# Kernel optimization log

Hardware: AMD Instinct MI355X
Metric: run time of the kernel (lower is better)

## Reference

```python
import jax, jax.numpy as jnp
import numpy as np

N_HEAD = 4

def setup_inputs() -> dict:
    key = jax.random.key(0)
    ks = jax.random.split(key, 10)
    B, N, C = 4, 16384, 256
    s = 1.0 / np.sqrt(C)
    inp = {
        'x': jax.random.normal(ks[0], (B, N, C), dtype=jnp.float32),
        'mask_x': jnp.ones((B, N), dtype=jnp.float32),
        'mask_y': jnp.ones((B, N), dtype=jnp.float32),
        'Wq': jax.random.normal(ks[1], (C, C), dtype=jnp.float32) * s,
        'bq': jnp.zeros((C,), dtype=jnp.float32),
        'Wk': jax.random.normal(ks[2], (C, C), dtype=jnp.float32) * s,
        'bk': jnp.zeros((C,), dtype=jnp.float32),
        'Wv': jax.random.normal(ks[3], (C, C), dtype=jnp.float32) * s,
        'bv': jnp.zeros((C,), dtype=jnp.float32),
        'Wp': jax.random.normal(ks[4], (C, C), dtype=jnp.float32) * s,
        'bp': jnp.zeros((C,), dtype=jnp.float32),
    }
    return inp

def reference(x, mask_x, mask_y, Wq, bq, Wk, bk, Wv, bv, Wp, bp):
    B, N, C = x.shape
    H = N_HEAD
    D = C // H
    # projections (y = x, self-attention path); weights stored [in, out]
    def split_heads(t):  # [B,N,C] -> [B,H,N,D]
        return t.reshape(B, N, H, D).transpose(0, 2, 1, 3)
    Q = split_heads(x @ Wq + bq)
    K = split_heads(x @ Wk + bk)
    V = split_heads(x @ Wv + bv)
    mx = mask_x[:, None, :, None]  # [B,1,N,1]
    my = mask_y[:, None, :, None]  # [B,1,M,1]
    K = K * my
    V = V * my
    # torch F.gelu default is exact (erf) gelu
    Q = jax.nn.gelu(Q, approximate=False) + 1.0
    K = jax.nn.gelu(K, approximate=False) + 1.0
    KV = jnp.einsum('bhmd,bhme->bhde', K, V)          # [B,H,D,D]
    K_sum = K.sum(axis=2, keepdims=True)               # [B,H,1,D]
    denom = jnp.sum(Q * K_sum, axis=-1, keepdims=True) # [B,H,N,1]
    attn_out = jnp.einsum('bhnd,bhde->bhne', Q, KV) / denom
    attn_out = attn_out * mx
    out = attn_out.transpose(0, 2, 1, 3).reshape(B, N, C)
    return out @ Wp + bp
```

## Files before the change

kernel.cpp:

```cpp
#include <hip/hip_runtime.h>
#include <hip/hip_bf16.h>
#include <cstdint>
#include <cstddef>

#define SEQ   16384
#define CHN   256

typedef __attribute__((ext_vector_type(8))) short  short8;
typedef __attribute__((ext_vector_type(4))) float  f32x4;

#define AS1 __attribute__((address_space(1)))
#define AS3 __attribute__((address_space(3)))
static __device__ __forceinline__ void gl_lds16(const void* g, void* l) {
    __builtin_amdgcn_global_load_lds((const AS1 void*)g, (AS3 void*)l, 16, 0, 0);
}

static __device__ __forceinline__ unsigned short f2bf(float f) {
    unsigned int u = __builtin_bit_cast(unsigned int, f);
    u += 0x7fffu + ((u >> 16) & 1u);
    return (unsigned short)(u >> 16);
}
static __device__ __forceinline__ float bf2f(unsigned short h) {
    unsigned int u = ((unsigned int)h) << 16;
    return __builtin_bit_cast(float, u);
}
static __device__ __forceinline__ float gelu_exact(float x) {
    return 0.5f * x * (1.0f + erff(x * 0.70710678118654752f));
}
static __device__ __forceinline__ int swz_us(int row, int kbyte) {
    return (row * 128 + (kbyte ^ ((row & 7) << 4))) >> 1;
}

__global__ __launch_bounds__(256) void cvt_kernel(
    const float* __restrict__ x, unsigned short* __restrict__ xb)
{
    const int t0 = blockIdx.x * 256 + threadIdx.x;
    #pragma unroll
    for (int i = 0; i < 4; ++i) {
        const long g = (long)t0 + (long)i * 524288;
        const float4 a = *(const float4*)(x + g * 8);
        const float4 b = *(const float4*)(x + g * 8 + 4);
        uint4 pk;
        pk.x = (unsigned int)f2bf(a.x) | ((unsigned int)f2bf(a.y) << 16);
        pk.y = (unsigned int)f2bf(a.z) | ((unsigned int)f2bf(a.w) << 16);
        pk.z = (unsigned int)f2bf(b.x) | ((unsigned int)f2bf(b.y) << 16);
        pk.w = (unsigned int)f2bf(b.z) | ((unsigned int)f2bf(b.w) << 16);
        *(uint4*)(xb + g * 8) = pk;
    }
}

__global__ __launch_bounds__(256) void prep_kernel(
    const float* __restrict__ Wq, const float* __restrict__ Wk,
    const float* __restrict__ Wv, const float* __restrict__ Wp,
    unsigned short* __restrict__ Wcat, unsigned short* __restrict__ Wpt,
    float* __restrict__ KV, float* __restrict__ Ksum)
{
    const int idx = blockIdx.x * 256 + threadIdx.x;
    const int n = idx >> 8, k = idx & 255;
    const int src = k * 256 + n;
    Wcat[idx]          = f2bf(Wq[src]);
    Wcat[65536 + idx]  = f2bf(Wk[src]);
    Wcat[131072 + idx] = f2bf(Wv[src]);
    Wpt[idx]           = f2bf(Wp[src]);
    KV[idx] = 0.0f;
    if (idx < 1024) Ksum[idx] = 0.0f;
}

__global__ __launch_bounds__(256) void qkv_gemm(
    const unsigned short* __restrict__ xb, const float* __restrict__ my,
    const unsigned short* __restrict__ Wcat,
    const float* __restrict__ bq, const float* __restrict__ bk,
    const float* __restrict__ bv,
    unsigned short* __restrict__ Qb, unsigned short* __restrict__ Kb,
    unsigned short* __restrict__ Vb)
{
    __shared__ unsigned short As[128 * 64];
    __shared__ unsigned short Bs[128 * 64];
    __shared__ float mys[128];
    const int t = threadIdx.x;
    const int nwg = 3072, phys = blockIdx.x;
    const int l = (phys & 7) * (nwg >> 3) + (phys >> 3);
    const int rt = l / 6, ct = l % 6;
    const long row0 = (long)rt * 128;
    const int  ncol0 = ct * 128;
    const int  mat = ct >> 1;
    const int lane = t & 63, wave = t >> 6, wm = wave >> 1, wn = wave & 1;

    if (t < 128) mys[t] = my[row0 + t];

    f32x4 acc[4][4];
    #pragma unroll
    for (int i = 0; i < 4; ++i)
        #pragma unroll
        for (int j = 0; j < 4; ++j) acc[i][j] = (f32x4)0.0f;

    for (int k0 = 0; k0 < 256; k0 += 64) {
        #pragma unroll
        for (int i = 0; i < 4; ++i) {
            const int c = i * 256 + t;
            gl_lds16(xb + (row0 + (c >> 3)) * 256 + k0 + (c & 7) * 8, &As[c * 8]);
        }
        #pragma unroll
        for (int i = 0; i < 4; ++i) {
            const int c = i * 256 + t;
            gl_lds16(Wcat + (size_t)(ncol0 + (c >> 3)) * 256 + k0 + (c & 7) * 8, &Bs[c * 8]);
        }
        __syncthreads();
        #pragma unroll
        for (int kk = 0; kk < 2; ++kk) {
            short8 af[4], bfr[4];
            #pragma unroll
            for (int mi = 0; mi < 4; ++mi) {
                const int r = wm * 64 + mi * 16 + (lane & 15);
                af[mi] = *(const short8*)&As[r * 64 + kk * 32 + (lane >> 4) * 8];
            }
            #pragma unroll
            for (int ni = 0; ni < 4; ++ni) {
                const int n = wn * 64 + ni * 16 + (lane & 15);
                bfr[ni] = *(const short8*)&Bs[n * 64 + kk * 32 + (lane >> 4) * 8];
            }
            #pragma unroll
            for (int mi = 0; mi < 4; ++mi)
                #pragma unroll
                for (int ni = 0; ni < 4; ++ni)
                    acc[mi][ni] = __builtin_amdgcn_mfma_f32_16x16x32_bf16(
                        af[mi], bfr[ni], acc[mi][ni], 0, 0, 0);
        }
        __syncthreads();
    }

    const float* bias  = (mat == 0) ? bq : (mat == 1) ? bk : bv;
    unsigned short* Ob = (mat == 0) ? Qb : (mat == 1) ? Kb : Vb;
    const int col0 = (ct & 1) * 128;
    #pragma unroll
    for (int ni = 0; ni < 4; ++ni) {
        const int coll = col0 + wn * 64 + ni * 16 + (lane & 15);
        const float bc = bias[coll];
        #pragma unroll
        for (int mi = 0; mi < 4; ++mi) {
            const int lr0 = wm * 64 + mi * 16 + ((lane >> 4) << 2);
            #pragma unroll
            for (int r = 0; r < 4; ++r) {
                const int lr = lr0 + r;
                float val = acc[mi][ni][r] + bc;
                if (mat == 0)      val = gelu_exact(val) + 1.0f;
                else if (mat == 1) val = gelu_exact(val * mys[lr]) + 1.0f;
                else               val = val * mys[lr];
                Ob[(row0 + lr) * 256 + coll] = f2bf(val);
            }
        }
    }
}

__global__ __launch_bounds__(256) void kv_reduce(
    const unsigned short* __restrict__ Kb, const unsigned short* __restrict__ Vb,
    float* __restrict__ KV, float* __restrict__ Ksum)
{
    __shared__ float kf[16][64];
    __shared__ float vf[16][64];
    const int t = threadIdx.x;
    const int bh = blockIdx.y;
    const long base = (long)(bh >> 2) * SEQ * 256 + (bh & 3) * 64;
    const long m0 = (long)blockIdx.x * 256;
    const int d0 = (t >> 4) * 4, e0 = (t & 15) * 4;
    const int sr = t >> 4, swhich = (t >> 3) & 1, sseg = t & 7;
    float acc[4][4] = {};
    float ks[4] = {};
    for (int it = 0; it < 16; ++it) {
        const long row = m0 + it * 16 + sr;
        const unsigned short* src = (swhich ? Vb : Kb) + base + row * 256 + sseg * 8;
        const uint4 raw = *(const uint4*)src;
        const unsigned short* rh = (const unsigned short*)&raw;
        float* dst = swhich ? &vf[sr][sseg * 8] : &kf[sr][sseg * 8];
        #pragma unroll
        for (int j = 0; j < 8; ++j) dst[j] = bf2f(rh[j]);
        __syncthreads();
        #pragma unroll
        for (int mm = 0; mm < 16; ++mm) {
            const float4 kd = *(const float4*)&kf[mm][d0];
            const float4 ve = *(const float4*)&vf[mm][e0];
            const float k4[4] = {kd.x, kd.y, kd.z, kd.w};
            const float v4[4] = {ve.x, ve.y, ve.z, ve.w};
            #pragma unroll
            for (int i = 0; i < 4; ++i)
                #pragma unroll
                for (int j = 0; j < 4; ++j) acc[i][j] += k4[i] * v4[j];
            if ((t & 15) == 0) {
                #pragma unroll
                for (int i = 0; i < 4; ++i) ks[i] += k4[i];
            }
        }
        __syncthreads();
    }
    #pragma unroll
    for (int i = 0; i < 4; ++i)
        #pragma unroll
        for (int j = 0; j < 4; ++j)
            atomicAdd(&KV[((size_t)bh * 64 + d0 + i) * 64 + e0 + j], acc[i][j]);
    if ((t & 15) == 0) {
        #pragma unroll
        for (int i = 0; i < 4; ++i) atomicAdd(&Ksum[bh * 64 + d0 + i], ks[i]);
    }
}

__global__ __launch_bounds__(256) void attn_kernel(
    const unsigned short* __restrict__ Qb, const float* __restrict__ KV,
    const float* __restrict__ Ksum, const float* __restrict__ mx,
    unsigned short* __restrict__ Ab)
{
    __shared__ unsigned short Qs[128 * 64];
    __shared__ unsigned short KVT[64 * 64];
    __shared__ float ksh[64];
    __shared__ float sden[128];
    const int t = threadIdx.x;
    const long row0 = (long)blockIdx.x * 128;
    const int b = (int)(row0 >> 14);
    const int lane = t & 63, wave = t >> 6, wm = wave >> 1, wn = wave & 1;

    for (int h = 0; h < 4; ++h) {
        const int bh = b * 4 + h;
        #pragma unroll
        for (int it = 0; it < 4; ++it) {
            const int idx = it * 256 + t;
            const int r = idx >> 3, c8 = (idx & 7) * 8;
            const uint4 v = *(const uint4*)(Qb + (row0 + r) * 256 + h * 64 + c8);
            *(uint4*)&Qs[swz_us(r, c8 * 2)] = v;
        }
        {
            const int e = t & 63, dg = t >> 6;
            #pragma unroll
            for (int i = 0; i < 16; ++i) {
                const int d = dg * 16 + i;
                const float v = KV[((size_t)bh * 64 + d) * 64 + e];
                KVT[(e * 128 + ((d * 2) ^ ((e & 7) << 4))) >> 1] = f2bf(v);
            }
        }
        if (t < 64) ksh[t] = Ksum[bh * 64 + t];
        __syncthreads();
        if (t < 128) {
            float s = 0.0f;
            for (int d = 0; d < 64; ++d)
                s += bf2f(Qs[swz_us(t, d * 2)]) * ksh[d];
            sden[t] = mx[row0 + t] / s;
        }
        __syncthreads();
        f32x4 acc[4][2];
        #pragma unroll
        for (int i = 0; i < 4; ++i) { acc[i][0] = (f32x4)0.0f; acc[i][1] = (f32x4)0.0f; }
        #pragma unroll
        for (int kk = 0; kk < 2; ++kk) {
            const int kbyte = kk * 64 + (lane >> 4) * 16;
            short8 af[4], bfr[2];
            #pragma unroll
            for (int mi = 0; mi < 4; ++mi) {
                const int r = wm * 64 + mi * 16 + (lane & 15);
                af[mi] = *(const short8*)&Qs[swz_us(r, kbyte)];
            }
            #pragma unroll
            for (int ni = 0; ni < 2; ++ni) {
                const int e = wn * 32 + ni * 16 + (lane & 15);
                bfr[ni] = *(const short8*)&KVT[swz_us(e, kbyte)];
            }
            #pragma unroll
            for (int mi = 0; mi < 4; ++mi)
                #pragma unroll
                for (int ni = 0; ni < 2; ++ni)
                    acc[mi][ni] = __builtin_amdgcn_mfma_f32_16x16x32_bf16(
                        af[mi], bfr[ni], acc[mi][ni], 0, 0, 0);
        }
        #pragma unroll
        for (int ni = 0; ni < 2; ++ni) {
            const int e = wn * 32 + ni * 16 + (lane & 15);
            #pragma unroll
            for (int mi = 0; mi < 4; ++mi) {
                const int lr0 = wm * 64 + mi * 16 + ((lane >> 4) << 2);
                #pragma unroll
                for (int r = 0; r < 4; ++r) {
                    const int lr = lr0 + r;
                    const float val = acc[mi][ni][r] * sden[lr];
                    Ab[(row0 + lr) * 256 + h * 64 + e] = f2bf(val);
                }
            }
        }
        __syncthreads();
    }
}

__global__ __launch_bounds__(256) void proj_gemm(
    const unsigned short* __restrict__ Ab, const unsigned short* __restrict__ Wpt,
    const float* __restrict__ bp, float* __restrict__ out)
{
    __shared__ unsigned short As[128 * 64];
    __shared__ unsigned short Bs[128 * 64];
    const int t = threadIdx.x;
    const int nwg = 1024, phys = blockIdx.x;
    const int l = (phys & 7) * (nwg >> 3) + (phys >> 3);
    const int rt = l >> 1, ct = l & 1;
    const long row0 = (long)rt * 128;
    const int col0 = ct * 128;
    const int lane = t & 63, wave = t >> 6, wm = wave >> 1, wn = wave & 1;

    f32x4 acc[4][4];
    #pragma unroll
    for (int i = 0; i < 4; ++i)
        #pragma unroll
        for (int j = 0; j < 4; ++j) acc[i][j] = (f32x4)0.0f;

    for (int k0 = 0; k0 < 256; k0 += 64) {
        #pragma unroll
        for (int i = 0; i < 4; ++i) {
            const int c = i * 256 + t;
            gl_lds16(Ab + (row0 + (c >> 3)) * 256 + k0 + (c & 7) * 8, &As[c * 8]);
        }
        #pragma unroll
        for (int i = 0; i < 4; ++i) {
            const int c = i * 256 + t;
            gl_lds16(Wpt + (size_t)(col0 + (c >> 3)) * 256 + k0 + (c & 7) * 8, &Bs[c * 8]);
        }
        __syncthreads();
        #pragma unroll
        for (int kk = 0; kk < 2; ++kk) {
            short8 af[4], bfr[4];
            #pragma unroll
            for (int mi = 0; mi < 4; ++mi) {
                const int r = wm * 64 + mi * 16 + (lane & 15);
                af[mi] = *(const short8*)&As[r * 64 + kk * 32 + (lane >> 4) * 8];
            }
            #pragma unroll
            for (int ni = 0; ni < 4; ++ni) {
                const int n = wn * 64 + ni * 16 + (lane & 15);
                bfr[ni] = *(const short8*)&Bs[n * 64 + kk * 32 + (lane >> 4) * 8];
            }
            #pragma unroll
            for (int mi = 0; mi < 4; ++mi)
                #pragma unroll
                for (int ni = 0; ni < 4; ++ni)
                    acc[mi][ni] = __builtin_amdgcn_mfma_f32_16x16x32_bf16(
                        af[mi], bfr[ni], acc[mi][ni], 0, 0, 0);
        }
        __syncthreads();
    }
    #pragma unroll
    for (int ni = 0; ni < 4; ++ni) {
        const int coll = col0 + wn * 64 + ni * 16 + (lane & 15);
        const float bc = bp[coll];
        #pragma unroll
        for (int mi = 0; mi < 4; ++mi) {
            const int lr0 = wm * 64 + mi * 16 + ((lane >> 4) << 2);
            #pragma unroll
            for (int r = 0; r < 4; ++r) {
                const long grow = row0 + lr0 + r;
                out[grow * 256 + coll] = acc[mi][ni][r] + bc;
            }
        }
    }
}

extern "C" void kernel_launch(void* const* d_in, const int* in_sizes, int n_in,
                              void* d_out, int out_size, void* d_ws, size_t ws_size,
                              hipStream_t stream)
{
    (void)in_sizes; (void)n_in; (void)out_size; (void)ws_size;
    const float* x  = (const float*)d_in[0];
    const float* mx = (const float*)d_in[1];
    const float* my = (const float*)d_in[2];
    const float* Wq = (const float*)d_in[3];
    const float* bq = (const float*)d_in[4];
    const float* Wk = (const float*)d_in[5];
    const float* bk = (const float*)d_in[6];
    const float* Wv = (const float*)d_in[7];
    const float* bv = (const float*)d_in[8];
    const float* Wp = (const float*)d_in[9];
    const float* bp = (const float*)d_in[10];
    float* out = (float*)d_out;

    const size_t nelem = (size_t)4 * SEQ * CHN;
    char* w = (char*)d_ws;
    unsigned short* xb   = (unsigned short*)w; w += nelem * 2;
    unsigned short* Qb   = (unsigned short*)w; w += nelem * 2;
    unsigned short* Kb   = (unsigned short*)w; w += nelem * 2;
    unsigned short* Vb   = (unsigned short*)w; w += nelem * 2;
    unsigned short* Wcat = (unsigned short*)w; w += 768 * 256 * 2;
    unsigned short* Wpt  = (unsigned short*)w; w += 131072;
    float* KV   = (float*)w; w += 262144;
    float* Ksum = (float*)w; w += 4096;
    unsigned short* Ab = Kb;

    cvt_kernel<<<2048, 256, 0, stream>>>(x, xb);
    prep_kernel<<<256, 256, 0, stream>>>(Wq, Wk, Wv, Wp, Wcat, Wpt, KV, Ksum);
    qkv_gemm<<<3072, 256, 0, stream>>>(xb, my, Wcat, bq, bk, bv, Qb, Kb, Vb);
    kv_reduce<<<dim3(64, 16), 256, 0, stream>>>(Kb, Vb, KV, Ksum);
    attn_kernel<<<512, 256, 0, stream>>>(Qb, KV, Ksum, mx, Ab);
    proj_gemm<<<1024, 256, 0, stream>>>(Ab, Wpt, bp, out);
}
```

Before: 349.9 us.

## Double-buffer and swizzle GEMMs, transpose K/V, compute KV with MFMA

The QKV and projection GEMMs now double-buffer their LDS tiles and use an XOR swizzle, so loads overlap MFMA work and LDS bank conflicts drop. The QKV epilogue stages results in LDS and writes vectorized rows; K and V are written transposed as [B,H,D,N]. This lets the KV reduction run as an MFMA GEMM instead of a scalar FP32 outer-product loop. The attention denominator is also computed with vectorized loads over all threads. The cost is more LDS per block and a transposed-store epilogue.

After: 338.1 us. 3.4% less time.

```diff
diff --git a/kernel.cpp b/kernel.cpp
--- a/kernel.cpp
+++ b/kernel.cpp
@@ -71,11 +71,11 @@
     const unsigned short* __restrict__ Wcat,
     const float* __restrict__ bq, const float* __restrict__ bk,
     const float* __restrict__ bv,
-    unsigned short* __restrict__ Qb, unsigned short* __restrict__ Kb,
-    unsigned short* __restrict__ Vb)
-{
-    __shared__ unsigned short As[128 * 64];
-    __shared__ unsigned short Bs[128 * 64];
+    unsigned short* __restrict__ Qb, unsigned short* __restrict__ Kt,
+    unsigned short* __restrict__ Vt)
+{
+    __shared__ unsigned short As[2][128 * 64];
+    __shared__ unsigned short Bs[2][128 * 64];
     __shared__ float mys[128];
     const int t = threadIdx.x;
     const int nwg = 3072, phys = blockIdx.x;
@@ -84,40 +84,52 @@
     const long row0 = (long)rt * 128;
     const int  ncol0 = ct * 128;
     const int  mat = ct >> 1;
+    const int  col0 = (ct & 1) * 128;
     const int lane = t & 63, wave = t >> 6, wm = wave >> 1, wn = wave & 1;
 
-    if (t < 128) mys[t] = my[row0 + t];
-
-    f32x4 acc[4][4];
-    #pragma unroll
-    for (int i = 0; i < 4; ++i)
-        #pragma unroll
-        for (int j = 0; j < 4; ++j) acc[i][j] = (f32x4)0.0f;
-
-    for (int k0 = 0; k0 < 256; k0 += 64) {
+    auto stage = [&](int buf, int k0) {
         #pragma unroll
         for (int i = 0; i < 4; ++i) {
             const int c = i * 256 + t;
-            gl_lds16(xb + (row0 + (c >> 3)) * 256 + k0 + (c & 7) * 8, &As[c * 8]);
+            const int row = c >> 3, j = (c & 7) ^ (row & 7);
+            gl_lds16(xb + (row0 + row) * 256 + k0 + j * 8, &As[buf][c * 8]);
         }
         #pragma unroll
         for (int i = 0; i < 4; ++i) {
             const int c = i * 256 + t;
-            gl_lds16(Wcat + (size_t)(ncol0 + (c >> 3)) * 256 + k0 + (c & 7) * 8, &Bs[c * 8]);
-        }
-        __syncthreads();
+            const int row = c >> 3, j = (c & 7) ^ (row & 7);
+            gl_lds16(Wcat + (size_t)(ncol0 + row) * 256 + k0 + j * 8, &Bs[buf][c * 8]);
+        }
+    };
+
+    if (t < 128) mys[t] = my[row0 + t];
+
+    f32x4 acc[4][4];
+    #pragma unroll
+    for (int i = 0; i < 4; ++i)
+        #pragma unroll
+        for (int j = 0; j < 4; ++j) acc[i][j] = (f32x4)0.0f;
+
+    stage(0, 0);
+    __syncthreads();
+
+    #pragma unroll
+    for (int s = 0; s < 4; ++s) {
+        const int buf = s & 1;
+        if (s < 3) stage(buf ^ 1, (s + 1) * 64);
         #pragma unroll
         for (int kk = 0; kk < 2; ++kk) {
+            const int g = kk * 4 + (lane >> 4);
             short8 af[4], bfr[4];
             #pragma unroll
             for (int mi = 0; mi < 4; ++mi) {
                 const int r = wm * 64 + mi * 16 + (lane & 15);
-                af[mi] = *(const short8*)&As[r * 64 + kk * 32 + (lane >> 4) * 8];
+                af[mi] = *(const short8*)&As[buf][r * 64 + (g ^ (r & 7)) * 8];
             }
             #pragma unroll
             for (int ni = 0; ni < 4; ++ni) {
                 const int n = wn * 64 + ni * 16 + (lane & 15);
-                bfr[ni] = *(const short8*)&Bs[n * 64 + kk * 32 + (lane >> 4) * 8];
+                bfr[ni] = *(const short8*)&Bs[buf][n * 64 + (g ^ (n & 7)) * 8];
             }
             #pragma unroll
             for (int mi = 0; mi < 4; ++mi)
@@ -129,13 +141,12 @@
         __syncthreads();
     }
 
-    const float* bias  = (mat == 0) ? bq : (mat == 1) ? bk : bv;
-    unsigned short* Ob = (mat == 0) ? Qb : (mat == 1) ? Kb : Vb;
-    const int col0 = (ct & 1) * 128;
+    unsigned short* C = &As[0][0];
+    const float* bias = (mat == 0) ? bq : (mat == 1) ? bk : bv;
     #pragma unroll
     for (int ni = 0; ni < 4; ++ni) {
-        const int coll = col0 + wn * 64 + ni * 16 + (lane & 15);
-        const float bc = bias[coll];
+        const int cl = wn * 64 + ni * 16 + (lane & 15);
+        const float bc = bias[col0 + cl];
         #pragma unroll
         for (int mi = 0; mi < 4; ++mi) {
             const int lr0 = wm * 64 + mi * 16 + ((lane >> 4) << 2);
@@ -146,61 +157,71 @@
                 if (mat == 0)      val = gelu_exact(val) + 1.0f;
                 else if (mat == 1) val = gelu_exact(val * mys[lr]) + 1.0f;
                 else               val = val * mys[lr];
-                Ob[(row0 + lr) * 256 + coll] = f2bf(val);
-            }
-        }
-    }
-}
-
-__global__ __launch_bounds__(256) void kv_reduce(
-    const unsigned short* __restrict__ Kb, const unsigned short* __restrict__ Vb,
+                if (mat == 0) {
+                    C[lr * 128 + cl] = f2bf(val);
+                } else {
+                    C[(cl * 256 + ((lr * 2) ^ ((cl & 7) << 4))) >> 1] = f2bf(val);
+                }
+            }
+        }
+    }
+    __syncthreads();
+
+    if (mat == 0) {
+        const int r = t >> 1, c0 = (t & 1) * 64;
+        uint4* dst = (uint4*)(Qb + (row0 + r) * 256 + col0 + c0);
+        const uint4* src = (const uint4*)&C[r * 128 + c0];
+        #pragma unroll
+        for (int q = 0; q < 8; ++q) dst[q] = src[q];
+    } else {
+        const int chl = t >> 1, mh = (t & 1) * 64;
+        const int chg = col0 + chl, h = chg >> 6, d = chg & 63;
+        const int b = (int)(row0 >> 14);
+        const long m0 = (row0 & 16383) + mh;
+        unsigned short* dstp = (mat == 1 ? Kt : Vt)
+                             + ((size_t)(b * 4 + h) * 64 + d) * SEQ + m0;
+        #pragma unroll
+        for (int q = 0; q < 8; ++q) {
+            const int byteoff = chl * 256 + ((mh * 2 + q * 16) ^ ((chl & 7) << 4));
+            *(uint4*)(dstp + q * 8) = *(const uint4*)((const char*)C + byteoff);
+        }
+    }
+}
+
+__global__ __launch_bounds__(256) void kv_gemm(
+    const unsigned short* __restrict__ Kt, const unsigned short* __restrict__ Vt,
     float* __restrict__ KV, float* __restrict__ Ksum)
 {
-    __shared__ float kf[16][64];
-    __shared__ float vf[16][64];
-    const int t = threadIdx.x;
+    const int t = threadIdx.x, lane = t & 63, w = t >> 6;
     const int bh = blockIdx.y;
-    const long base = (long)(bh >> 2) * SEQ * 256 + (bh & 3) * 64;
-    const long m0 = (long)blockIdx.x * 256;
-    const int d0 = (t >> 4) * 4, e0 = (t & 15) * 4;
-    const int sr = t >> 4, swhich = (t >> 3) & 1, sseg = t & 7;
-    float acc[4][4] = {};
-    float ks[4] = {};
-    for (int it = 0; it < 16; ++it) {
-        const long row = m0 + it * 16 + sr;
-        const unsigned short* src = (swhich ? Vb : Kb) + base + row * 256 + sseg * 8;
-        const uint4 raw = *(const uint4*)src;
-        const unsigned short* rh = (const unsigned short*)&raw;
-        float* dst = swhich ? &vf[sr][sseg * 8] : &kf[sr][sseg * 8];
-        #pragma unroll
-        for (int j = 0; j < 8; ++j) dst[j] = bf2f(rh[j]);
-        __syncthreads();
-        #pragma unroll
-        for (int mm = 0; mm < 16; ++mm) {
-            const float4 kd = *(const float4*)&kf[mm][d0];
-            const float4 ve = *(const float4*)&vf[mm][e0];
-            const float k4[4] = {kd.x, kd.y, kd.z, kd.w};
-            const float v4[4] = {ve.x, ve.y, ve.z, ve.w};
-            #pragma unroll
-            for (int i = 0; i < 4; ++i)
-                #pragma unroll
-                for (int j = 0; j < 4; ++j) acc[i][j] += k4[i] * v4[j];
-            if ((t & 15) == 0) {
-                #pragma unroll
-                for (int i = 0; i < 4; ++i) ks[i] += k4[i];
-            }
-        }
-        __syncthreads();
-    }
-    #pragma unroll
-    for (int i = 0; i < 4; ++i)
+    const long k0 = (long)blockIdx.x * 512;
+    const unsigned short* Ka = Kt + ((size_t)bh * 64 + w * 16 + (lane & 15)) * SEQ;
+    f32x4 acc[4];
+    #pragma unroll
+    for (int e = 0; e < 4; ++e) acc[e] = (f32x4)0.0f;
+    float ksacc = 0.0f;
+
+    for (int ks = 0; ks < 16; ++ks) {
+        const long kk = k0 + ks * 32 + (lane >> 4) * 8;
+        const short8 a = *(const short8*)(Ka + kk);
+        #pragma unroll
+        for (int j = 0; j < 8; ++j) ksacc += bf2f((unsigned short)a[j]);
+        #pragma unroll
+        for (int e = 0; e < 4; ++e) {
+            const short8 b = *(const short8*)(Vt
+                + ((size_t)bh * 64 + e * 16 + (lane & 15)) * SEQ + kk);
+            acc[e] = __builtin_amdgcn_mfma_f32_16x16x32_bf16(a, b, acc[e], 0, 0, 0);
+        }
+    }
+    ksacc += __shfl_xor(ksacc, 16, 64);
+    ksacc += __shfl_xor(ksacc, 32, 64);
+    if (lane < 16) atomicAdd(&Ksum[bh * 64 + w * 16 + lane], ksacc);
+    #pragma unroll
+    for (int e = 0; e < 4; ++e)
         #pragma unroll
         for (int j = 0; j < 4; ++j)
-            atomicAdd(&KV[((size_t)bh * 64 + d0 + i) * 64 + e0 + j], acc[i][j]);
-    if ((t & 15) == 0) {
-        #pragma unroll
-        for (int i = 0; i < 4; ++i) atomicAdd(&Ksum[bh * 64 + d0 + i], ks[i]);
-    }
+            atomicAdd(&KV[((size_t)bh * 64 + w * 16 + (lane >> 4) * 4 + j) * 64
+                          + e * 16 + (lane & 15)], acc[e][j]);
 }
 
 __global__ __launch_bounds__(256) void attn_kernel(
@@ -237,11 +258,19 @@
         }
         if (t < 64) ksh[t] = Ksum[bh * 64 + t];
         __syncthreads();
-        if (t < 128) {
+        {
+            const int r = t >> 1, hf = t & 1;
             float s = 0.0f;
-            for (int d = 0; d < 64; ++d)
-                s += bf2f(Qs[swz_us(t, d * 2)]) * ksh[d];
-            sden[t] = mx[row0 + t] / s;
+            #pragma unroll
+            for (int c8 = 0; c8 < 4; ++c8) {
+                const int ke = hf * 32 + c8 * 8;
+                const short8 q8 = *(const short8*)&Qs[swz_us(r, ke * 2)];
+                #pragma unroll
+                for (int j = 0; j < 8; ++j)
+                    s += bf2f((unsigned short)q8[j]) * ksh[ke + j];
+            }
+            s += __shfl_xor(s, 1, 64);
+            if (hf == 0) sden[r] = mx[row0 + r] / s;
         }
         __syncthreads();
         f32x4 acc[4][2];
@@ -290,8 +319,8 @@
     const unsigned short* __restrict__ Ab, const unsigned short* __restrict__ Wpt,
     const float* __restrict__ bp, float* __restrict__ out)
 {
-    __shared__ unsigned short As[128 * 64];
-    __shared__ unsigned short Bs[128 * 64];
+    __shared__ unsigned short As[2][128 * 64];
+    __shared__ unsigned short Bs[2][128 * 64];
     const int t = threadIdx.x;
     const int nwg = 1024, phys = blockIdx.x;
     const int l = (phys & 7) * (nwg >> 3) + (phys >> 3);
@@ -300,36 +329,47 @@
     const int col0 = ct * 128;
     const int lane = t & 63, wave = t >> 6, wm = wave >> 1, wn = wave & 1;
 
-    f32x4 acc[4][4];
-    #pragma unroll
-    for (int i = 0; i < 4; ++i)
-        #pragma unroll
-        for (int j = 0; j < 4; ++j) acc[i][j] = (f32x4)0.0f;
-
-    for (int k0 = 0; k0 < 256; k0 += 64) {
+    auto stage = [&](int buf, int k0) {
         #pragma unroll
         for (int i = 0; i < 4; ++i) {
             const int c = i * 256 + t;
-            gl_lds16(Ab + (row0 + (c >> 3)) * 256 + k0 + (c & 7) * 8, &As[c * 8]);
+            const int row = c >> 3, j = (c & 7) ^ (row & 7);
+            gl_lds16(Ab + (row0 + row) * 256 + k0 + j * 8, &As[buf][c * 8]);
         }
         #pragma unroll
         for (int i = 0; i < 4; ++i) {
             const int c = i * 256 + t;
-            gl_lds16(Wpt + (size_t)(col0 + (c >> 3)) * 256 + k0 + (c & 7) * 8, &Bs[c * 8]);
-        }
-        __syncthreads();
+            const int row = c >> 3, j = (c & 7) ^ (row & 7);
+            gl_lds16(Wpt + (size_t)(col0 + row) * 256 + k0 + j * 8, &Bs[buf][c * 8]);
+        }
+    };
+
+    f32x4 acc[4][4];
+    #pragma unroll
+    for (int i = 0; i < 4; ++i)
+        #pragma unroll
+        for (int j = 0; j < 4; ++j) acc[i][j] = (f32x4)0.0f;
+
+    stage(0, 0);
+    __syncthreads();
+
+    #pragma unroll
+    for (int s = 0; s < 4; ++s) {
+        const int buf = s & 1;
+        if (s < 3) stage(buf ^ 1, (s + 1) * 64);
         #pragma unroll
         for (int kk = 0; kk < 2; ++kk) {
+            const int g = kk * 4 + (lane >> 4);
             short8 af[4], bfr[4];
             #pragma unroll
             for (int mi = 0; mi < 4; ++mi) {
                 const int r = wm * 64 + mi * 16 + (lane & 15);
-                af[mi] = *(const short8*)&As[r * 64 + kk * 32 + (lane >> 4) * 8];
+                af[mi] = *(const short8*)&As[buf][r * 64 + (g ^ (r & 7)) * 8];
             }
             #pragma unroll
             for (int ni = 0; ni < 4; ++ni) {
                 const int n = wn * 64 + ni * 16 + (lane & 15);
-                bfr[ni] = *(const short8*)&Bs[n * 64 + kk * 32 + (lane >> 4) * 8];
+                bfr[ni] = *(const short8*)&Bs[buf][n * 64 + (g ^ (n & 7)) * 8];
             }
             #pragma unroll
             for (int mi = 0; mi < 4; ++mi)
@@ -378,18 +418,18 @@
     char* w = (char*)d_ws;
     unsigned short* xb   = (unsigned short*)w; w += nelem * 2;
     unsigned short* Qb   = (unsigned short*)w; w += nelem * 2;
-    unsigned short* Kb   = (unsigned short*)w; w += nelem * 2;
-    unsigned short* Vb   = (unsigned short*)w; w += nelem * 2;
+    unsigned short* Kt   = (unsigned short*)w; w += nelem * 2;
+    unsigned short* Vt   = (unsigned short*)w; w += nelem * 2;
     unsigned short* Wcat = (unsigned short*)w; w += 768 * 256 * 2;
     unsigned short* Wpt  = (unsigned short*)w; w += 131072;
     float* KV   = (float*)w; w += 262144;
     float* Ksum = (float*)w; w += 4096;
-    unsigned short* Ab = Kb;
+    unsigned short* Ab = Kt;
 
     cvt_kernel<<<2048, 256, 0, stream>>>(x, xb);
     prep_kernel<<<256, 256, 0, stream>>>(Wq, Wk, Wv, Wp, Wcat, Wpt, KV, Ksum);
-    qkv_gemm<<<3072, 256, 0, stream>>>(xb, my, Wcat, bq, bk, bv, Qb, Kb, Vb);
-    kv_reduce<<<dim3(64, 16), 256, 0, stream>>>(Kb, Vb, KV, Ksum);
+    qkv_gemm<<<3072, 256, 0, stream>>>(xb, my, Wcat, bq, bk, bv, Qb, Kt, Vt);
+    kv_gemm<<<dim3(32, 16), 256, 0, stream>>>(Kt, Vt, KV, Ksum);
     attn_kernel<<<512, 256, 0, stream>>>(Qb, KV, Ksum, mx, Ab);
     proj_gemm<<<1024, 256, 0, stream>>>(Ab, Wpt, bp, out);
 }
```
